# Performance work log

Measured on AMD Instinct MI355X. Metric: run time of the kernel, lower is better.

Reference implementation:

```python
import jax, jax.numpy as jnp
import numpy as np

N, D, H, E = 4096, 512, 8, 131072
DH = D // H
BN_EPS = 1e-5


def setup_inputs() -> dict:
    key = jax.random.key(0)
    ks = jax.random.split(key, 12)
    def w(k, shape):
        return jax.random.normal(k, shape, dtype=jnp.float32) * 0.02
    return {
        'x': jax.random.normal(ks[0], (N, D), dtype=jnp.float32),
        'edge_index': jax.random.randint(ks[1], (2, E), 0, N),
        'edge_attr': jax.random.normal(ks[2], (E, D), dtype=jnp.float32),
        # GINE MLP: Linear(D,D) -> ReLU -> Linear(D,D)  (torch layout [out,in])
        'w_gin1': w(ks[3], (D, D)), 'b_gin1': jnp.zeros((D,), jnp.float32),
        'w_gin2': w(ks[4], (D, D)), 'b_gin2': jnp.zeros((D,), jnp.float32),
        # MultiheadAttention in/out projections
        'w_qkv': w(ks[5], (3 * D, D)), 'b_qkv': jnp.zeros((3 * D,), jnp.float32),
        'w_o': w(ks[6], (D, D)), 'b_o': jnp.zeros((D,), jnp.float32),
        # BatchNorm affine params
        'bn1l_g': jnp.ones((D,), jnp.float32), 'bn1l_b': jnp.zeros((D,), jnp.float32),
        'bn1a_g': jnp.ones((D,), jnp.float32), 'bn1a_b': jnp.zeros((D,), jnp.float32),
        # FFN: D -> 2D -> D
        'w_ff1': w(ks[7], (2 * D, D)), 'b_ff1': jnp.zeros((2 * D,), jnp.float32),
        'w_ff2': w(ks[8], (D, 2 * D)), 'b_ff2': jnp.zeros((D,), jnp.float32),
        'bn2_g': jnp.ones((D,), jnp.float32), 'bn2_b': jnp.zeros((D,), jnp.float32),
    }


def _bn(x, g, b):
    # BatchNorm1d in training mode: batch statistics over the node dim
    m = jnp.mean(x, axis=0)
    v = jnp.var(x, axis=0)
    return (x - m) * jax.lax.rsqrt(v + BN_EPS) * g + b


def _forward(x, edge_index, edge_attr,
             w_gin1, b_gin1, w_gin2, b_gin2,
             w_qkv, b_qkv, w_o, b_o,
             bn1l_g, bn1l_b, bn1a_g, bn1a_b,
             w_ff1, b_ff1, w_ff2, b_ff2, bn2_g, bn2_b):
    h_in = x
    src, dst = edge_index[0], edge_index[1]
    # --- local GINEConv: nn((1+eps)*x + sum_j relu(x_j + e_ji)), eps=0 ---
    msg = jax.nn.relu(x[src] + edge_attr)                       # [E, D]
    agg = jax.ops.segment_sum(msg, dst, num_segments=N)         # [N, D]
    gin_h = x + agg
    h_local = jax.nn.relu(gin_h @ w_gin1.T + b_gin1) @ w_gin2.T + b_gin2
    h_local = _bn(h_in + h_local, bn1l_g, bn1l_b)               # residual + BN
    # --- global multi-head self-attention over all nodes (single graph) ---
    qkv = x @ w_qkv.T + b_qkv                                   # [N, 3D]
    q, k, v = jnp.split(qkv, 3, axis=-1)
    q = q.reshape(N, H, DH).transpose(1, 0, 2)                  # [H, N, DH]
    k = k.reshape(N, H, DH).transpose(1, 0, 2)
    v = v.reshape(N, H, DH).transpose(1, 0, 2)
    scores = jnp.einsum('hnd,hmd->hnm', q, k) / np.float32(np.sqrt(DH))
    attn = jax.nn.softmax(scores, axis=-1)                      # [H, N, N]
    o = jnp.einsum('hnm,hmd->hnd', attn, v).transpose(1, 0, 2).reshape(N, D)
    h_attn = _bn(h_in + (o @ w_o.T + b_o), bn1a_g, bn1a_b)
    # --- combine branches + FFN block ---
    h = h_local + h_attn
    h = h + (jax.nn.relu(h @ w_ff1.T + b_ff1) @ w_ff2.T + b_ff2)
    return _bn(h, bn2_g, bn2_b)


def reference(x, edge_index, edge_attr,
              w_gin1, b_gin1, w_gin2, b_gin2,
              w_qkv, b_qkv, w_o, b_o,
              bn1l_g, bn1l_b, bn1a_g, bn1a_b,
              w_ff1, b_ff1, w_ff2, b_ff2, bn2_g, bn2_b):
    return _forward(x, edge_index, edge_attr,
                    w_gin1, b_gin1, w_gin2, b_gin2,
                    w_qkv, b_qkv, w_o, b_o,
                    bn1l_g, bn1l_b, bn1a_g, bn1a_b,
                    w_ff1, b_ff1, w_ff2, b_ff2, bn2_g, bn2_b)
```

## Files before the change

### kernel.cpp

```cpp
#include <hip/hip_runtime.h>

#define Nn 4096
#define Dd 512
#define Hh 8
#define Ee 131072
#define DEGCAP 96

typedef __attribute__((ext_vector_type(8))) short short8v;
typedef __attribute__((ext_vector_type(4))) short short4v;
typedef __attribute__((ext_vector_type(4))) float f32x4v;
typedef __attribute__((ext_vector_type(4))) unsigned short ushort4v;

__device__ __forceinline__ float bf2f(unsigned short u) {
    return __uint_as_float(((unsigned int)u) << 16);
}
__device__ __forceinline__ unsigned short f2bf(float f) {
    unsigned int u = __float_as_uint(f);
    return (unsigned short)((u + 0x7fff + ((u >> 16) & 1)) >> 16);
}
__device__ __forceinline__ void gl_lds16(const void* g, void* l) {
    __builtin_amdgcn_global_load_lds((const __attribute__((address_space(1))) void*)g,
                                     (__attribute__((address_space(3))) void*)l, 16, 0, 0);
}

struct CastJobs {
    const float* src[7];
    unsigned short* dst[7];
    int start[8];
    int* cnt;
    float* stats;
};

__global__ __launch_bounds__(256) void cast_multi(CastJobs cj) {
    int gid = blockIdx.x * 256 + threadIdx.x;
    if (gid < 4096) cj.cnt[gid] = 0;
    if (gid < 6144) cj.stats[gid] = 0.f;
    int b = blockIdx.x;
    int j = 0;
    while (b >= cj.start[j + 1]) j++;
    int off = (b - cj.start[j]) * 1024 + threadIdx.x * 4;
    f32x4v v = *(const f32x4v*)(cj.src[j] + off);
    ushort4v o;
    o.x = f2bf(v.x); o.y = f2bf(v.y); o.z = f2bf(v.z); o.w = f2bf(v.w);
    *(ushort4v*)(cj.dst[j] + off) = o;
}

__global__ __launch_bounds__(256) void edge_scatter(const int* __restrict__ ei,
                                                    int* __restrict__ cnt,
                                                    int* __restrict__ eidx) {
    int e = blockIdx.x * 256 + threadIdx.x;
    int d = ei[Ee + e];
    int pos = atomicAdd(&cnt[d], 1);
    if (pos < DEGCAP) eidx[d * DEGCAP + pos] = e;
}

__global__ __launch_bounds__(256) void gine_gather(const float* __restrict__ x,
                                                   const int* __restrict__ ei,
                                                   const float* __restrict__ ea,
                                                   const int* __restrict__ cnt,
                                                   const int* __restrict__ eidx,
                                                   unsigned short* __restrict__ gh) {
    __shared__ int se[DEGCAP];
    __shared__ int ss[DEGCAP];
    __shared__ float part[512];
    const int node = blockIdx.x;
    const int t = threadIdx.x;
    const int deg = min(cnt[node], DEGCAP);
    const int tc = t & 127, ep = t >> 7;

    if (t < deg) {
        int e = eidx[node * DEGCAP + t];
        se[t] = e;
        ss[t] = ei[e];
    }
    __syncthreads();

    f32x4v acc = {0.f, 0.f, 0.f, 0.f};
    int k = ep;
    while (k + 2 < deg) {
        int e0 = se[k], s0 = ss[k];
        int e1 = se[k + 2], s1 = ss[k + 2];
        f32x4v ev0 = *(const f32x4v*)(ea + (size_t)e0 * Dd + tc * 4);
        f32x4v xv0 = *(const f32x4v*)(x + (size_t)s0 * Dd + tc * 4);
        f32x4v ev1 = *(const f32x4v*)(ea + (size_t)e1 * Dd + tc * 4);
        f32x4v xv1 = *(const f32x4v*)(x + (size_t)s1 * Dd + tc * 4);
#pragma unroll
        for (int i = 0; i < 4; i++) {
            acc[i] += fmaxf(xv0[i] + ev0[i], 0.f);
            acc[i] += fmaxf(xv1[i] + ev1[i], 0.f);
        }
        k += 4;
    }
    if (k < deg) {
        int e0 = se[k], s0 = ss[k];
        f32x4v ev0 = *(const f32x4v*)(ea + (size_t)e0 * Dd + tc * 4);
        f32x4v xv0 = *(const f32x4v*)(x + (size_t)s0 * Dd + tc * 4);
#pragma unroll
        for (int i = 0; i < 4; i++) acc[i] += fmaxf(xv0[i] + ev0[i], 0.f);
    }

    if (ep) *(f32x4v*)&part[tc * 4] = acc;
    __syncthreads();
    if (!ep) {
        f32x4v o = *(const f32x4v*)&part[tc * 4];
        f32x4v xd = *(const f32x4v*)(x + (size_t)node * Dd + tc * 4);
        ushort4v ov;
#pragma unroll
        for (int i = 0; i < 4; i++) ov[i] = f2bf(xd[i] + acc[i] + o[i]);
        *(ushort4v*)(gh + (size_t)node * Dd + tc * 4) = ov;
    }
}

template <int K, int MB, bool RELU, bool OUTBF16, bool ADDRES>
__global__ __launch_bounds__(256) void gemm_bt(const short* __restrict__ A,
                                               const short* __restrict__ B,
                                               const float* __restrict__ bias,
                                               const float* __restrict__ res,
                                               void* __restrict__ outp, int Nc) {
    constexpr int BM = MB * 32;
    __shared__ alignas(16) short lA[BM * 32];
    __shared__ alignas(16) short lB[128 * 32];
    const int t = threadIdx.x;
    const int lane = t & 63, w = t >> 6;
    const int wr = w >> 1, wc = w & 1;
    const int l15 = lane & 15, lhi = lane >> 4;
    const int m0 = blockIdx.y * BM, n0 = blockIdx.x * 128;
    f32x4v acc[MB][4] = {};
    const int c0 = t, c1 = t + 256;

    for (int k0 = 0; k0 < K; k0 += 32) {
        __syncthreads();
        gl_lds16(A + (size_t)(m0 + (c0 >> 2)) * K + k0 + (c0 & 3) * 8, (char*)lA + c0 * 16);
        if constexpr (MB == 4)
            gl_lds16(A + (size_t)(m0 + (c1 >> 2)) * K + k0 + (c1 & 3) * 8, (char*)lA + c1 * 16);
        gl_lds16(B + (size_t)(n0 + (c0 >> 2)) * K + k0 + (c0 & 3) * 8, (char*)lB + c0 * 16);
        gl_lds16(B + (size_t)(n0 + (c1 >> 2)) * K + k0 + (c1 & 3) * 8, (char*)lB + c1 * 16);
        __syncthreads();
        short8v af[MB], bf[4];
#pragma unroll
        for (int m = 0; m < MB; m++)
            af[m] = *(const short8v*)&lA[(wr * (MB * 16) + m * 16 + l15) * 32 + lhi * 8];
#pragma unroll
        for (int n = 0; n < 4; n++)
            bf[n] = *(const short8v*)&lB[(wc * 64 + n * 16 + l15) * 32 + lhi * 8];
#pragma unroll
        for (int m = 0; m < MB; m++)
#pragma unroll
            for (int n = 0; n < 4; n++)
                acc[m][n] = __builtin_amdgcn_mfma_f32_16x16x32_bf16(af[m], bf[n], acc[m][n], 0, 0, 0);
    }

#pragma unroll
    for (int m = 0; m < MB; m++)
#pragma unroll
        for (int n = 0; n < 4; n++)
#pragma unroll
            for (int j = 0; j < 4; j++) {
                int col = n0 + wc * 64 + n * 16 + l15;
                int row = m0 + wr * (MB * 16) + m * 16 + lhi * 4 + j;
                float v = acc[m][n][j] + bias[col];
                if (RELU) v = fmaxf(v, 0.f);
                if (ADDRES) v += res[(size_t)row * Nc + col];
                if (OUTBF16)
                    ((unsigned short*)outp)[(size_t)row * Nc + col] = f2bf(v);
                else
                    ((float*)outp)[(size_t)row * Nc + col] = v;
            }
}

__global__ __launch_bounds__(256) void attn_fwd(const short* __restrict__ qkv,
                                                float* __restrict__ opart0,
                                                float* __restrict__ opart1,
                                                float2* __restrict__ ml) {
    __shared__ alignas(16) short lK[2][64 * 64];
    __shared__ alignas(16) short lV[2][4 * 64 * 16];
    __shared__ alignas(16) short lP[4 * 2 * 16 * 64];
    const int t = threadIdx.x, lane = t & 63, w = t >> 6;
    const int h = blockIdx.y >> 1, half = blockIdx.y & 1;
    const int kvbase = half * 2048;
    const int qw = blockIdx.x * 128 + w * 32;
    const int l15 = lane & 15, lhi = lane >> 4;
    const int ksw = l15 & 7;
    const int qs3 = (l15 >> 1) & 7;
    float* __restrict__ opart = half ? opart1 : opart0;

    short* pP = lP + w * 2048;

    short8v qf[2][2];
#pragma unroll
    for (int g = 0; g < 2; g++)
#pragma unroll
        for (int kk = 0; kk < 2; kk++)
            qf[g][kk] = *(const short8v*)&qkv[(size_t)(qw + g * 16 + l15) * 1536 + h * 64 + kk * 32 + lhi * 8];

    f32x4v oacc[2][4] = {};
    float mrow[2] = {-1e30f, -1e30f}, lrow[2] = {0.f, 0.f};
    const float SC2 = 0.125f * 1.44269504f;
    const float THR_RAW = 44.3614f;

    int kidx[4][2];
#pragma unroll
    for (int r = 0; r < 4; r++)
#pragma unroll
        for (int kk = 0; kk < 2; kk++)
            kidx[r][kk] = (l15 + r * 16) * 64 + (((kk * 4 + lhi) ^ ksw) * 8);

    int pw_idx[4], prd_idx[2];
#pragma unroll
    for (int c2 = 0; c2 < 4; c2++)
        pw_idx[c2] = l15 * 64 + (((c2 * 2 + (lhi >> 1)) ^ qs3) * 8) + ((lhi & 1) * 4);
#pragma unroll
    for (int c = 0; c < 2; c++)
        prd_idx[c] = l15 * 64 + (((c * 4 + lhi) ^ qs3) * 8);

    unsigned vbase0 = (unsigned)(unsigned long long)&lV[0][0] + lhi * 256 + l15 * 2;

    auto stage = [&](int kt, int b) {
        int kv0 = kvbase + kt * 64;
#pragma unroll
        for (int i = 0; i < 2; i++) {
            int row = (t >> 3) + 32 * i;
            gl_lds16(qkv + (size_t)(kv0 + row) * 1536 + 512 + h * 64 + ((t & 7) ^ ((t >> 3) & 7)) * 8,
                     (char*)&lK[b][0] + t * 16 + i * 4096);
        }
#pragma unroll
        for (int i = 0; i < 2; i++) {
            int db = (t >> 7) + 2 * i;
            int kv = (t >> 1) & 63;
            int dh_in = (t & 1) * 8;
            gl_lds16(qkv + (size_t)(kv0 + kv) * 1536 + 1024 + h * 64 + db * 16 + dh_in,
                     (char*)&lV[b][0] + t * 16 + i * 4096);
        }
    };

    stage(0, 0);
    __syncthreads();

    for (int kt = 0; kt < 32; kt++) {
        const int b = kt & 1;
        if (kt + 1 < 32) stage(kt + 1, b ^ 1);

        const short* Kb = &lK[b][0];
        const unsigned vbase = vbase0 + b * 8192;

        f32x4v s0[4] = {}, s1[4] = {};
        __builtin_amdgcn_s_setprio(1);
#pragma unroll
        for (int r = 0; r < 4; r++) {
            short8v k0 = *(const short8v*)&Kb[kidx[r][0]];
            short8v k1 = *(const short8v*)&Kb[kidx[r][1]];
            s0[r] = __builtin_amdgcn_mfma_f32_16x16x32_bf16(k0, qf[0][0], s0[r], 0, 0, 0);
            s0[r] = __builtin_amdgcn_mfma_f32_16x16x32_bf16(k1, qf[0][1], s0[r], 0, 0, 0);
            s1[r] = __builtin_amdgcn_mfma_f32_16x16x32_bf16(k0, qf[1][0], s1[r], 0, 0, 0);
            s1[r] = __builtin_amdgcn_mfma_f32_16x16x32_bf16(k1, qf[1][1], s1[r], 0, 0, 0);
        }
        __builtin_amdgcn_s_setprio(0);

#pragma unroll
        for (int g = 0; g < 2; g++) {
            f32x4v* s = g ? s1 : s0;
            float m8 = s[0][0];
#pragma unroll
            for (int r = 0; r < 4; r++)
#pragma unroll
                for (int j = 0; j < 4; j++) m8 = fmaxf(m8, s[r][j]);
            m8 = fmaxf(m8, __shfl_xor(m8, 16));
            m8 = fmaxf(m8, __shfl_xor(m8, 32));
            if (!__all(m8 - mrow[g] <= THR_RAW)) {
                float mnew = fmaxf(mrow[g], m8);
                float sc = exp2f((mrow[g] - mnew) * SC2);
                lrow[g] *= sc;
                mrow[g] = mnew;
#pragma unroll
                for (int j = 0; j < 4; j++) {
                    float scj = __shfl(sc, lhi * 4 + j);
#pragma unroll
                    for (int n = 0; n < 4; n++) oacc[g][n][j] *= scj;
                }
            }
            float mS = mrow[g] * SC2;
            float p[16];
            float rs = 0.f;
#pragma unroll
            for (int r = 0; r < 4; r++)
#pragma unroll
                for (int j = 0; j < 4; j++) {
                    float e = exp2f(fmaf(s[r][j], SC2, -mS));
                    p[r * 4 + j] = e;
                    rs += e;
                }
            rs += __shfl_xor(rs, 16);
            rs += __shfl_xor(rs, 32);
            lrow[g] += rs;

            short* pPg = pP + g * 1024;
#pragma unroll
            for (int c2 = 0; c2 < 4; c2++) {
                short4v pk;
#pragma unroll
                for (int j = 0; j < 4; j++) pk[j] = (short)f2bf(p[c2 * 4 + j]);
                *(short4v*)&pPg[pw_idx[c2]] = pk;
            }
        }
        asm volatile("" ::: "memory");

        short8v pf[2][2];
#pragma unroll
        for (int g = 0; g < 2; g++)
#pragma unroll
            for (int c = 0; c < 2; c++)
                pf[g][c] = *(const short8v*)&pP[g * 1024 + prd_idx[c]];

        short4v v00a, v00b, v01a, v01b, v10a, v10b, v11a, v11b;
        short4v v20a, v20b, v21a, v21b, v30a, v30b, v31a, v31b;
        asm volatile("ds_read_b64_tr_b16 %0, %1" : "=v"(v00a) : "v"(vbase));
        asm volatile("ds_read_b64_tr_b16 %0, %1 offset:128" : "=v"(v00b) : "v"(vbase));
        asm volatile("ds_read_b64_tr_b16 %0, %1 offset:1024" : "=v"(v01a) : "v"(vbase));
        asm volatile("ds_read_b64_tr_b16 %0, %1 offset:1152" : "=v"(v01b) : "v"(vbase));
        asm volatile("ds_read_b64_tr_b16 %0, %1 offset:2048" : "=v"(v10a) : "v"(vbase));
        asm volatile("ds_read_b64_tr_b16 %0, %1 offset:2176" : "=v"(v10b) : "v"(vbase));
        asm volatile("ds_read_b64_tr_b16 %0, %1 offset:3072" : "=v"(v11a) : "v"(vbase));
        asm volatile("ds_read_b64_tr_b16 %0, %1 offset:3200" : "=v"(v11b) : "v"(vbase));
        asm volatile("ds_read_b64_tr_b16 %0, %1 offset:4096" : "=v"(v20a) : "v"(vbase));
        asm volatile("ds_read_b64_tr_b16 %0, %1 offset:4224" : "=v"(v20b) : "v"(vbase));
        asm volatile("ds_read_b64_tr_b16 %0, %1 offset:5120" : "=v"(v21a) : "v"(vbase));
        asm volatile("ds_read_b64_tr_b16 %0, %1 offset:5248" : "=v"(v21b) : "v"(vbase));
        asm volatile("ds_read_b64_tr_b16 %0, %1 offset:6144" : "=v"(v30a) : "v"(vbase));
        asm volatile("ds_read_b64_tr_b16 %0, %1 offset:6272" : "=v"(v30b) : "v"(vbase));
        asm volatile("ds_read_b64_tr_b16 %0, %1 offset:7168" : "=v"(v31a) : "v"(vbase));
        asm volatile("ds_read_b64_tr_b16 %0, %1 offset:7296" : "=v"(v31b) : "v"(vbase));

        asm volatile("s_waitcnt lgkmcnt(0)" ::: "memory");
        __builtin_amdgcn_sched_barrier(0);

#define VFCAT(a, b) __builtin_shufflevector(a, b, 0, 1, 2, 3, 4, 5, 6, 7)
        short8v vv[4][2];
        vv[0][0] = VFCAT(v00a, v00b); vv[0][1] = VFCAT(v01a, v01b);
        vv[1][0] = VFCAT(v10a, v10b); vv[1][1] = VFCAT(v11a, v11b);
        vv[2][0] = VFCAT(v20a, v20b); vv[2][1] = VFCAT(v21a, v21b);
        vv[3][0] = VFCAT(v30a, v30b); vv[3][1] = VFCAT(v31a, v31b);
#undef VFCAT
        __builtin_amdgcn_s_setprio(1);
#pragma unroll
        for (int g = 0; g < 2; g++)
#pragma unroll
            for (int n = 0; n < 4; n++) {
                oacc[g][n] = __builtin_amdgcn_mfma_f32_16x16x32_bf16(pf[g][0], vv[n][0], oacc[g][n], 0, 0, 0);
                oacc[g][n] = __builtin_amdgcn_mfma_f32_16x16x32_bf16(pf[g][1], vv[n][1], oacc[g][n], 0, 0, 0);
            }
        __builtin_amdgcn_s_setprio(0);

        __syncthreads();
    }

#pragma unroll
    for (int g = 0; g < 2; g++) {
#pragma unroll
        for (int j = 0; j < 4; j++) {
            int row = qw + g * 16 + lhi * 4 + j;
#pragma unroll
            for (int n = 0; n < 4; n++)
                opart[(size_t)row * Dd + h * 64 + n * 16 + l15] = oacc[g][n][j];
        }
        if (lhi == 0)
            ml[(size_t)(half * Hh + h) * Nn + qw + g * 16 + l15] = make_float2(mrow[g], lrow[g]);
    }
}

__global__ __launch_bounds__(256) void attn_combine(const float* __restrict__ o0,
                                                    const float* __restrict__ o1,
                                                    const float2* __restrict__ ml,
                                                    unsigned short* __restrict__ ob) {
    const float SC2 = 0.125f * 1.44269504f;
    int idx = (blockIdx.x * 256 + threadIdx.x) * 4;
    int row = idx >> 9, col = idx & 511, h = col >> 6;
    float2 a = ml[(size_t)h * Nn + row];
    float2 b = ml[(size_t)(Hh + h) * Nn + row];
    float m = fmaxf(a.x, b.x);
    float e1 = exp2f((a.x - m) * SC2);
    float e2 = exp2f((b.x - m) * SC2);
    float inv = 1.f / (a.y * e1 + b.y * e2);
    f32x4v n1 = *(const f32x4v*)(o0 + idx);
    f32x4v n2 = *(const f32x4v*)(o1 + idx);
    ushort4v o;
#pragma unroll
    for (int e = 0; e < 4; e++) o[e] = f2bf((n1[e] * e1 + n2[e] * e2) * inv);
    *(ushort4v*)(ob + idx) = o;
}

__global__ __launch_bounds__(256) void colstats2(const float* __restrict__ x,
                                                 const float* __restrict__ p1,
                                                 const float* __restrict__ p2,
                                                 float* __restrict__ stats) {
    __shared__ float buf[256];
    int t = threadIdx.x;
    int strip = blockIdx.x & 7, chunk = blockIdx.x >> 3;
    int col = strip * 64 + (t & 63);
    int r0 = chunk * 128 + (t >> 6);
    float sa = 0, qa = 0, sb = 0, qb = 0;
    for (int i = 0; i < 32; i++) {
        size_t idx = (size_t)(r0 + i * 4) * Dd + col;
        float xx = x[idx];
        float a = xx + p1[idx];
        float b = xx + p2[idx];
        sa += a; qa += a * a; sb += b; qb += b * b;
    }
    float vals[4] = {sa, qa, sb, qb};
    for (int s = 0; s < 4; s++) {
        __syncthreads();
        buf[t] = vals[s];
        __syncthreads();
        if (t < 64) {
            float tot = buf[t] + buf[t + 64] + buf[t + 128] + buf[t + 192];
            atomicAdd(&stats[s * 512 + strip * 64 + t], tot);
        }
    }
}

__global__ __launch_bounds__(256) void colstats1(const float* __restrict__ p,
                                                 float* __restrict__ stats) {
    __shared__ float buf[256];
    int t = threadIdx.x;
    int strip = blockIdx.x & 7, chunk = blockIdx.x >> 3;
    int col = strip * 64 + (t & 63);
    int r0 = chunk * 128 + (t >> 6);
    float sa = 0, qa = 0;
    for (int i = 0; i < 32; i++) {
        float a = p[(size_t)(r0 + i * 4) * Dd + col];
        sa += a; qa += a * a;
    }
    float vals[2] = {sa, qa};
    for (int s = 0; s < 2; s++) {
        __syncthreads();
        buf[t] = vals[s];
        __syncthreads();
        if (t < 64) {
            float tot = buf[t] + buf[t + 64] + buf[t + 128] + buf[t + 192];
            atomicAdd(&stats[4096 + s * 512 + strip * 64 + t], tot);
        }
    }
}

__global__ __launch_bounds__(256) void bn_combine(const float* __restrict__ x,
                                                  const float* __restrict__ p1,
                                                  const float* __restrict__ p2,
                                                  const float* __restrict__ stats,
                                                  const float* __restrict__ g1,
                                                  const float* __restrict__ b1,
                                                  const float* __restrict__ g2,
                                                  const float* __restrict__ b2,
                                                  float* __restrict__ h,
                                                  unsigned short* __restrict__ hb) {
    int i0 = (blockIdx.x * 256 + threadIdx.x) * 4;
    int c0 = i0 & 511;
    f32x4v xv = *(const f32x4v*)(x + i0);
    f32x4v av = *(const f32x4v*)(p1 + i0);
    f32x4v bv = *(const f32x4v*)(p2 + i0);
    f32x4v hv;
    ushort4v hbv;
#pragma unroll
    for (int e = 0; e < 4; e++) {
        int c = c0 + e;
        float ma = stats[c] * (1.f / Nn);
        float va = stats[512 + c] * (1.f / Nn) - ma * ma;
        float sA = g1[c] * rsqrtf(va + 1e-5f);
        float bA = b1[c] - ma * sA;
        float mb = stats[1024 + c] * (1.f / Nn);
        float vb = stats[1536 + c] * (1.f / Nn) - mb * mb;
        float sB = g2[c] * rsqrtf(vb + 1e-5f);
        float bB = b2[c] - mb * sB;
        float a = xv[e] + av[e];
        float b = xv[e] + bv[e];
        float val = a * sA + bA + b * sB + bB;
        hv[e] = val;
        hbv[e] = f2bf(val);
    }
    *(f32x4v*)(h + i0) = hv;
    *(ushort4v*)(hb + i0) = hbv;
}

__global__ __launch_bounds__(256) void bn_apply(float* __restrict__ out,
                                                const float* __restrict__ stats,
                                                const float* __restrict__ g,
                                                const float* __restrict__ b) {
    int i0 = (blockIdx.x * 256 + threadIdx.x) * 4;
    int c0 = i0 & 511;
    f32x4v v = *(const f32x4v*)(out + i0);
#pragma unroll
    for (int e = 0; e < 4; e++) {
        int c = c0 + e;
        float m = stats[4096 + c] * (1.f / Nn);
        float va = stats[4608 + c] * (1.f / Nn) - m * m;
        float s = g[c] * rsqrtf(va + 1e-5f);
        v[e] = (v[e] - m) * s + b[c];
    }
    *(f32x4v*)(out + i0) = v;
}

extern "C" void kernel_launch(void* const* d_in, const int* in_sizes, int n_in,
                              void* d_out, int out_size, void* d_ws, size_t ws_size,
                              hipStream_t stream) {
    const float* x = (const float*)d_in[0];
    const int* ei = (const int*)d_in[1];
    const float* ea = (const float*)d_in[2];
    const float* w_gin1 = (const float*)d_in[3];
    const float* b_gin1 = (const float*)d_in[4];
    const float* w_gin2 = (const float*)d_in[5];
    const float* b_gin2 = (const float*)d_in[6];
    const float* w_qkv = (const float*)d_in[7];
    const float* b_qkv = (const float*)d_in[8];
    const float* w_o = (const float*)d_in[9];
    const float* b_o = (const float*)d_in[10];
    const float* bn1l_g = (const float*)d_in[11];
    const float* bn1l_b = (const float*)d_in[12];
    const float* bn1a_g = (const float*)d_in[13];
    const float* bn1a_b = (const float*)d_in[14];
    const float* w_ff1 = (const float*)d_in[15];
    const float* b_ff1 = (const float*)d_in[16];
    const float* w_ff2 = (const float*)d_in[17];
    const float* b_ff2 = (const float*)d_in[18];
    const float* bn2_g = (const float*)d_in[19];
    const float* bn2_b = (const float*)d_in[20];

    char* ws = (char*)d_ws;
    unsigned short* wg1b = (unsigned short*)(ws + 0);
    unsigned short* wg2b = (unsigned short*)(ws + 524288);
    unsigned short* wqkvb = (unsigned short*)(ws + 1048576);
    unsigned short* wob = (unsigned short*)(ws + 2621440);
    unsigned short* wf1b = (unsigned short*)(ws + 3145728);
    unsigned short* wf2b = (unsigned short*)(ws + 4194304);
    unsigned short* xb = (unsigned short*)(ws + 5242880);
    unsigned short* qkvb = (unsigned short*)(ws + 9437184);
    int* eidx = (int*)(ws + 22020096);
    int* cnt = (int*)(ws + 23592960);
    unsigned short* ginh = (unsigned short*)(ws + 30408704);
    float2* ml = (float2*)(ws + 30408704);
    unsigned short* t1 = (unsigned short*)(ws + 34603008);
    float* hlp = (float*)(ws + 38797312);
    unsigned short* obuf = (unsigned short*)(ws + 47185920);
    float* attn_pre = (float*)(ws + 51380224);
    float* hbuf = (float*)(ws + 59768832);
    float* opart0 = (float*)(ws + 59768832);
    unsigned short* hb = (unsigned short*)(ws + 68157440);
    unsigned short* t2 = (unsigned short*)(ws + 72351744);
    float* opart1 = (float*)(ws + 72351744);
    float* stats = (float*)(ws + 80740352);

    CastJobs cj;
    cj.src[0] = x;      cj.dst[0] = xb;
    cj.src[1] = w_gin1; cj.dst[1] = wg1b;
    cj.src[2] = w_gin2; cj.dst[2] = wg2b;
    cj.src[3] = w_qkv;  cj.dst[3] = wqkvb;
    cj.src[4] = w_o;    cj.dst[4] = wob;
    cj.src[5] = w_ff1;  cj.dst[5] = wf1b;
    cj.src[6] = w_ff2;  cj.dst[6] = wf2b;
    cj.cnt = cnt;
    cj.stats = stats;
    int nelem[7] = {Nn * Dd, Dd * Dd, Dd * Dd, 3 * Dd * Dd, Dd * Dd, 2 * Dd * Dd, 2 * Dd * Dd};
    cj.start[0] = 0;
    for (int i = 0; i < 7; i++) cj.start[i + 1] = cj.start[i] + nelem[i] / 1024;
    cast_multi<<<cj.start[7], 256, 0, stream>>>(cj);

    edge_scatter<<<Ee / 256, 256, 0, stream>>>(ei, cnt, eidx);
    gine_gather<<<Nn, 256, 0, stream>>>(x, ei, ea, cnt, eidx, ginh);

    gemm_bt<512, 2, true, true, false><<<dim3(4, 64), 256, 0, stream>>>(
        (const short*)ginh, (const short*)wg1b, b_gin1, nullptr, t1, 512);
    gemm_bt<512, 2, false, false, false><<<dim3(4, 64), 256, 0, stream>>>(
        (const short*)t1, (const short*)wg2b, b_gin2, nullptr, hlp, 512);

    gemm_bt<512, 4, false, true, false><<<dim3(12, 32), 256, 0, stream>>>(
        (const short*)xb, (const short*)wqkvb, b_qkv, nullptr, qkvb, 1536);
    attn_fwd<<<dim3(Nn / 128, Hh * 2), 256, 0, stream>>>((const short*)qkvb, opart0, opart1, ml);
    attn_combine<<<Nn * Dd / 1024, 256, 0, stream>>>(opart0, opart1, ml, obuf);
    gemm_bt<512, 2, false, false, false><<<dim3(4, 64), 256, 0, stream>>>(
        (const short*)obuf, (const short*)wob, b_o, nullptr, attn_pre, 512);

    colstats2<<<256, 256, 0, stream>>>(x, hlp, attn_pre, stats);
    bn_combine<<<Nn * Dd / 1024, 256, 0, stream>>>(x, hlp, attn_pre, stats,
                                                   bn1l_g, bn1l_b, bn1a_g, bn1a_b, hbuf, hb);

    gemm_bt<512, 4, true, true, false><<<dim3(8, 32), 256, 0, stream>>>(
        (const short*)hb, (const short*)wf1b, b_ff1, nullptr, t2, 1024);
    gemm_bt<1024, 2, false, false, true><<<dim3(4, 64), 256, 0, stream>>>(
        (const short*)t2, (const short*)wf2b, b_ff2, hbuf, d_out, 512);

    colstats1<<<256, 256, 0, stream>>>((const float*)d_out, stats);
    bn_apply<<<Nn * Dd / 1024, 256, 0, stream>>>((float*)d_out, stats, bn2_g, bn2_b);
}
```

Before: 295.2 us.

## Fuse BatchNorm column statistics into GEMM epilogues and store attention partials as bf16

```diff
diff --git a/kernel.cpp b/kernel.cpp
--- a/kernel.cpp
+++ b/kernel.cpp
@@ -111,12 +111,14 @@
     }
 }
 
-template <int K, int MB, bool RELU, bool OUTBF16, bool ADDRES>
+template <int K, int MB, bool RELU, bool OUTBF16, bool ADDRES, bool SXADD, int SOFF>
 __global__ __launch_bounds__(256) void gemm_bt(const short* __restrict__ A,
                                                const short* __restrict__ B,
                                                const float* __restrict__ bias,
                                                const float* __restrict__ res,
-                                               void* __restrict__ outp, int Nc) {
+                                               void* __restrict__ outp, int Nc,
+                                               const float* __restrict__ sx,
+                                               float* __restrict__ stats) {
     constexpr int BM = MB * 32;
     __shared__ alignas(16) short lA[BM * 32];
     __shared__ alignas(16) short lB[128 * 32];
@@ -150,6 +152,8 @@
                 acc[m][n] = __builtin_amdgcn_mfma_f32_16x16x32_bf16(af[m], bf[n], acc[m][n], 0, 0, 0);
     }
 
+    float csum[4] = {0.f, 0.f, 0.f, 0.f}, cssq[4] = {0.f, 0.f, 0.f, 0.f};
+
 #pragma unroll
     for (int m = 0; m < MB; m++)
 #pragma unroll
@@ -158,19 +162,45 @@
             for (int j = 0; j < 4; j++) {
                 int col = n0 + wc * 64 + n * 16 + l15;
                 int row = m0 + wr * (MB * 16) + m * 16 + lhi * 4 + j;
+                size_t idx = (size_t)row * Nc + col;
                 float v = acc[m][n][j] + bias[col];
                 if (RELU) v = fmaxf(v, 0.f);
-                if (ADDRES) v += res[(size_t)row * Nc + col];
+                if (ADDRES) v += res[idx];
+                if constexpr (SOFF >= 0) {
+                    float a = SXADD ? (sx[idx] + v) : v;
+                    csum[n] += a;
+                    cssq[n] += a * a;
+                }
                 if (OUTBF16)
-                    ((unsigned short*)outp)[(size_t)row * Nc + col] = f2bf(v);
+                    ((unsigned short*)outp)[idx] = f2bf(v);
                 else
-                    ((float*)outp)[(size_t)row * Nc + col] = v;
+                    ((float*)outp)[idx] = v;
             }
+
+    if constexpr (SOFF >= 0) {
+        __shared__ float sst[256];
+        sst[t] = 0.f;
+        __syncthreads();
+#pragma unroll
+        for (int n = 0; n < 4; n++) {
+            float s = csum[n], q = cssq[n];
+            s += __shfl_xor(s, 16); s += __shfl_xor(s, 32);
+            q += __shfl_xor(q, 16); q += __shfl_xor(q, 32);
+            if (lhi == 0) {
+                int c = wc * 64 + n * 16 + l15;
+                atomicAdd(&sst[c * 2], s);
+                atomicAdd(&sst[c * 2 + 1], q);
+            }
+        }
+        __syncthreads();
+        int c = t >> 1;
+        atomicAdd(&stats[SOFF + (t & 1) * 512 + n0 + c], sst[t]);
+    }
 }
 
 __global__ __launch_bounds__(256) void attn_fwd(const short* __restrict__ qkv,
-                                                float* __restrict__ opart0,
-                                                float* __restrict__ opart1,
+                                                unsigned short* __restrict__ opart0,
+                                                unsigned short* __restrict__ opart1,
                                                 float2* __restrict__ ml) {
     __shared__ alignas(16) short lK[2][64 * 64];
     __shared__ alignas(16) short lV[2][4 * 64 * 16];
@@ -182,7 +212,7 @@
     const int l15 = lane & 15, lhi = lane >> 4;
     const int ksw = l15 & 7;
     const int qs3 = (l15 >> 1) & 7;
-    float* __restrict__ opart = half ? opart1 : opart0;
+    unsigned short* __restrict__ opart = half ? opart1 : opart0;
 
     short* pP = lP + w * 2048;
 
@@ -360,15 +390,15 @@
             int row = qw + g * 16 + lhi * 4 + j;
 #pragma unroll
             for (int n = 0; n < 4; n++)
-                opart[(size_t)row * Dd + h * 64 + n * 16 + l15] = oacc[g][n][j];
+                opart[(size_t)row * Dd + h * 64 + n * 16 + l15] = f2bf(oacc[g][n][j]);
         }
         if (lhi == 0)
             ml[(size_t)(half * Hh + h) * Nn + qw + g * 16 + l15] = make_float2(mrow[g], lrow[g]);
     }
 }
 
-__global__ __launch_bounds__(256) void attn_combine(const float* __restrict__ o0,
-                                                    const float* __restrict__ o1,
+__global__ __launch_bounds__(256) void attn_combine(const unsigned short* __restrict__ o0,
+                                                    const unsigned short* __restrict__ o1,
                                                     const float2* __restrict__ ml,
                                                     unsigned short* __restrict__ ob) {
     const float SC2 = 0.125f * 1.44269504f;
@@ -380,65 +410,13 @@
     float e1 = exp2f((a.x - m) * SC2);
     float e2 = exp2f((b.x - m) * SC2);
     float inv = 1.f / (a.y * e1 + b.y * e2);
-    f32x4v n1 = *(const f32x4v*)(o0 + idx);
-    f32x4v n2 = *(const f32x4v*)(o1 + idx);
+    ushort4v n1 = *(const ushort4v*)(o0 + idx);
+    ushort4v n2 = *(const ushort4v*)(o1 + idx);
     ushort4v o;
 #pragma unroll
-    for (int e = 0; e < 4; e++) o[e] = f2bf((n1[e] * e1 + n2[e] * e2) * inv);
+    for (int e = 0; e < 4; e++)
+        o[e] = f2bf((bf2f(n1[e]) * e1 + bf2f(n2[e]) * e2) * inv);
     *(ushort4v*)(ob + idx) = o;
-}
-
-__global__ __launch_bounds__(256) void colstats2(const float* __restrict__ x,
-                                                 const float* __restrict__ p1,
-                                                 const float* __restrict__ p2,
-                                                 float* __restrict__ stats) {
-    __shared__ float buf[256];
-    int t = threadIdx.x;
-    int strip = blockIdx.x & 7, chunk = blockIdx.x >> 3;
-    int col = strip * 64 + (t & 63);
-    int r0 = chunk * 128 + (t >> 6);
-    float sa = 0, qa = 0, sb = 0, qb = 0;
-    for (int i = 0; i < 32; i++) {
-        size_t idx = (size_t)(r0 + i * 4) * Dd + col;
-        float xx = x[idx];
-        float a = xx + p1[idx];
-        float b = xx + p2[idx];
-        sa += a; qa += a * a; sb += b; qb += b * b;
-    }
-    float vals[4] = {sa, qa, sb, qb};
-    for (int s = 0; s < 4; s++) {
-        __syncthreads();
-        buf[t] = vals[s];
-        __syncthreads();
-        if (t < 64) {
-            float tot = buf[t] + buf[t + 64] + buf[t + 128] + buf[t + 192];
-            atomicAdd(&stats[s * 512 + strip * 64 + t], tot);
-        }
-    }
-}
-
-__global__ __launch_bounds__(256) void colstats1(const float* __restrict__ p,
-                                                 float* __restrict__ stats) {
-    __shared__ float buf[256];
-    int t = threadIdx.x;
-    int strip = blockIdx.x & 7, chunk = blockIdx.x >> 3;
-    int col = strip * 64 + (t & 63);
-    int r0 = chunk * 128 + (t >> 6);
-    float sa = 0, qa = 0;
-    for (int i = 0; i < 32; i++) {
-        float a = p[(size_t)(r0 + i * 4) * Dd + col];
-        sa += a; qa += a * a;
-    }
-    float vals[2] = {sa, qa};
-    for (int s = 0; s < 2; s++) {
-        __syncthreads();
-        buf[t] = vals[s];
-        __syncthreads();
-        if (t < 64) {
-            float tot = buf[t] + buf[t + 64] + buf[t + 128] + buf[t + 192];
-            atomicAdd(&stats[4096 + s * 512 + strip * 64 + t], tot);
-        }
-    }
 }
 
 __global__ __launch_bounds__(256) void bn_combine(const float* __restrict__ x,
@@ -540,10 +518,10 @@
     unsigned short* obuf = (unsigned short*)(ws + 47185920);
     float* attn_pre = (float*)(ws + 51380224);
     float* hbuf = (float*)(ws + 59768832);
-    float* opart0 = (float*)(ws + 59768832);
+    unsigned short* opart0 = (unsigned short*)(ws + 59768832);
     unsigned short* hb = (unsigned short*)(ws + 68157440);
     unsigned short* t2 = (unsigned short*)(ws + 72351744);
-    float* opart1 = (float*)(ws + 72351744);
+    unsigned short* opart1 = (unsigned short*)(ws + 72351744);
     float* stats = (float*)(ws + 80740352);
 
     CastJobs cj;
@@ -564,27 +542,25 @@
     edge_scatter<<<Ee / 256, 256, 0, stream>>>(ei, cnt, eidx);
     gine_gather<<<Nn, 256, 0, stream>>>(x, ei, ea, cnt, eidx, ginh);
 
-    gemm_bt<512, 2, true, true, false><<<dim3(4, 64), 256, 0, stream>>>(
-        (const short*)ginh, (const short*)wg1b, b_gin1, nullptr, t1, 512);
-    gemm_bt<512, 2, false, false, false><<<dim3(4, 64), 256, 0, stream>>>(
-        (const short*)t1, (const short*)wg2b, b_gin2, nullptr, hlp, 512);
-
-    gemm_bt<512, 4, false, true, false><<<dim3(12, 32), 256, 0, stream>>>(
-        (const short*)xb, (const short*)wqkvb, b_qkv, nullptr, qkvb, 1536);
+    gemm_bt<512, 2, true, true, false, false, -1><<<dim3(4, 64), 256, 0, stream>>>(
+        (const short*)ginh, (const short*)wg1b, b_gin1, nullptr, t1, 512, nullptr, nullptr);
+    gemm_bt<512, 2, false, false, false, true, 0><<<dim3(4, 64), 256, 0, stream>>>(
+        (const short*)t1, (const short*)wg2b, b_gin2, nullptr, hlp, 512, x, stats);
+
+    gemm_bt<512, 4, false, true, false, false, -1><<<dim3(12, 32), 256, 0, stream>>>(
+        (const short*)xb, (const short*)wqkvb, b_qkv, nullptr, qkvb, 1536, nullptr, nullptr);
     attn_fwd<<<dim3(Nn / 128, Hh * 2), 256, 0, stream>>>((const short*)qkvb, opart0, opart1, ml);
     attn_combine<<<Nn * Dd / 1024, 256, 0, stream>>>(opart0, opart1, ml, obuf);
-    gemm_bt<512, 2, false, false, false><<<dim3(4, 64), 256, 0, stream>>>(
-        (const short*)obuf, (const short*)wob, b_o, nullptr, attn_pre, 512);
-
-    colstats2<<<256, 256, 0, stream>>>(x, hlp, attn_pre, stats);
+    gemm_bt<512, 2, false, false, false, true, 1024><<<dim3(4, 64), 256, 0, stream>>>(
+        (const short*)obuf, (const short*)wob, b_o, nullptr, attn_pre, 512, x, stats);
+
     bn_combine<<<Nn * Dd / 1024, 256, 0, stream>>>(x, hlp, attn_pre, stats,
                                                    bn1l_g, bn1l_b, bn1a_g, bn1a_b, hbuf, hb);
 
-    gemm_bt<512, 4, true, true, false><<<dim3(8, 32), 256, 0, stream>>>(
-        (const short*)hb, (const short*)wf1b, b_ff1, nullptr, t2, 1024);
-    gemm_bt<1024, 2, false, false, true><<<dim3(4, 64), 256, 0, stream>>>(
-        (const short*)t2, (const short*)wf2b, b_ff2, hbuf, d_out, 512);
-
-    colstats1<<<256, 256, 0, stream>>>((const float*)d_out, stats);
+    gemm_bt<512, 4, true, true, false, false, -1><<<dim3(8, 32), 256, 0, stream>>>(
+        (const short*)hb, (const short*)wf1b, b_ff1, nullptr, t2, 1024, nullptr, nullptr);
+    gemm_bt<1024, 2, false, false, true, false, 4096><<<dim3(4, 64), 256, 0, stream>>>(
+        (const short*)t2, (const short*)wf2b, b_ff2, hbuf, d_out, 512, nullptr, stats);
+
     bn_apply<<<Nn * Dd / 1024, 256, 0, stream>>>((float*)d_out, stats, bn2_g, bn2_b);
 }
```

Result: no change. 292.8 us (-0.8%).
